# Performance work log

Hardware: AMD Instinct MI355X
Metric: run time of the kernel (lower is better)

Reference implementation:

```python
import jax, jax.numpy as jnp
import numpy as np

DIM = 256      # model dim E
H = 8          # num_heads
M = 32         # ball_size
TOPK = 2       # selected balls per query
N = 256        # number of balls
NM = N * M     # total points (8192)


def setup_inputs() -> dict:
    key = jax.random.key(0)
    k1, k2 = jax.random.split(key)
    x = jax.random.normal(k1, (NM, DIM), dtype=jnp.float32)
    pos = jax.random.normal(k2, (NM, 3), dtype=jnp.float32)
    return {"x": x, "pos": pos}


def reference(x, pos):
    e = DIM // H                      # per-head dim
    scale = DIM ** (-0.5)             # note: module scales by full dim, not head dim
    # pe_proj(compute_rel_pos(pos)) == 0 in the source (dead code), so x is unchanged.
    # qkv repeat + decompose '(H E K)' makes q == k == v == x reshaped per head.
    xh = x.reshape(N, M, H, e).transpose(0, 2, 1, 3)   # (n, H, m, e)
    q = xh
    k = xh
    v = xh

    # --- select_balls (runs under torch.no_grad) ---
    qf = jax.lax.stop_gradient(q).transpose(1, 0, 2, 3).reshape(H, NM, e)   # (H, nm, e)
    kmean = jax.lax.stop_gradient(k).mean(axis=2).transpose(1, 0, 2)        # (H, n, e)
    sim = jax.nn.softmax(jnp.einsum('hqe,hne->hqn', qf, kmean) * scale, axis=-1)
    topv, topi = jax.lax.top_k(sim, TOPK)               # (H, nm, topk)

    # straight-through gates (values were computed under no_grad -> constant 1.0)
    gates = topv + jax.lax.stop_gradient(1.0 - topv)
    # mask: each topk slot repeated over the m leaves of its ball
    fmask = jnp.repeat(topv > 1e-10, M, axis=-1)        # (H, nm, topk*m)

    # --- gather selected balls (avoid the torch repeat-then-gather blowup) ---
    kh = k.transpose(1, 0, 2, 3)                        # (H, n, m, e)
    vh = v.transpose(1, 0, 2, 3)
    gather = jax.vmap(lambda t, i: t[i])                # per-head fancy gather
    ksel = gather(kh, topi)                             # (H, nm, topk, m, e)
    vsel = gather(vh, topi)
    ksel = gates[..., None, None] * ksel                # use_diff_topk=True
    ksel = ksel.reshape(H, NM, TOPK * M, e)
    vsel = vsel.reshape(H, NM, TOPK * M, e)

    # --- masked attention over gathered keys ---
    qq = q.transpose(1, 0, 2, 3).reshape(H, NM, e)      # (H, nm, e)
    fsim = jnp.einsum('hqe,hqse->hqs', qq, ksel) * scale
    fsim = jnp.where(fmask, fsim, -jnp.finfo(fsim.dtype).max)
    attn = jax.nn.softmax(fsim, axis=-1)
    out = jnp.einsum('hqs,hqse->hqe', attn, vsel)       # (H, nm, e)
    return out.transpose(1, 0, 2).reshape(NM, DIM)      # (nm, H*e)
```

## Files before the change

kernel.cpp:

```cpp
#include <hip/hip_runtime.h>

#define FLT_BIG 3.402823466e38f

static __device__ __forceinline__ bool better(float v1, int i1, float v2, int i2) {
  return (v1 > v2) || ((v1 == v2) && (i1 < i2));
}

static __device__ __forceinline__ int xcd_swizzle(int nblocks) {
  const int bid = blockIdx.x;
  const int chunk = nblocks >> 3;
  return (bid & 7) * chunk + (bid >> 3);
}

__global__ void kmeanT_kernel(const float* __restrict__ x, float* __restrict__ kmT) {
  const int n = blockIdx.x;
  const int t = threadIdx.x;
  const float* base = x + n * 32 * 256 + t;
  float acc = 0.f;
  #pragma unroll
  for (int j = 0; j < 32; ++j) acc += base[j * 256];
  const int h = t >> 5, e = t & 31;
  kmT[h * 8192 + e * 256 + n] = acc * (1.0f / 32.0f);
}

__global__ __launch_bounds__(256) void select_kernel(const float* __restrict__ x,
                                                     const float* __restrict__ kmT,
                                                     int2* __restrict__ sel) {
  __shared__ float smem[32 * 260];
  const int vb = xcd_swizzle(2048);
  const int h = vb >> 8;
  const int qg = vb & 255;
  const int t = threadIdx.x;
  const int w = t >> 6, lane = t & 63;

  {
    const int r = t >> 3, c = t & 7;
    *(float4*)&smem[r * 32 + c * 4] =
        *(const float4*)(x + (qg * 32 + r) * 256 + h * 32 + c * 4);
  }
  __syncthreads();

  const float4* kmp = (const float4*)(kmT + h * 8192);
  float acc[8][4];
  #pragma unroll
  for (int qq = 0; qq < 8; ++qq)
    #pragma unroll
    for (int j = 0; j < 4; ++j) acc[qq][j] = 0.f;

  {
    float4 ka[4], kb[4];
    #pragma unroll
    for (int d = 0; d < 4; ++d) ka[d] = kmp[d * 64 + lane];

    #pragma unroll
    for (int e0 = 0; e0 < 8; ++e0) {
      float4* cur = (e0 & 1) ? kb : ka;
      float4* nxt = (e0 & 1) ? ka : kb;
      if (e0 < 7) {
        #pragma unroll
        for (int d = 0; d < 4; ++d) nxt[d] = kmp[((e0 + 1) * 4 + d) * 64 + lane];
      }
      #pragma unroll
      for (int qq = 0; qq < 8; ++qq) {
        const float4 qf = *(const float4*)&smem[(w * 8 + qq) * 32 + e0 * 4];
        acc[qq][0] = fmaf(qf.w, cur[3].x, fmaf(qf.z, cur[2].x, fmaf(qf.y, cur[1].x, fmaf(qf.x, cur[0].x, acc[qq][0]))));
        acc[qq][1] = fmaf(qf.w, cur[3].y, fmaf(qf.z, cur[2].y, fmaf(qf.y, cur[1].y, fmaf(qf.x, cur[0].y, acc[qq][1]))));
        acc[qq][2] = fmaf(qf.w, cur[3].z, fmaf(qf.z, cur[2].z, fmaf(qf.y, cur[1].z, fmaf(qf.x, cur[0].z, acc[qq][2]))));
        acc[qq][3] = fmaf(qf.w, cur[3].w, fmaf(qf.z, cur[2].w, fmaf(qf.y, cur[1].w, fmaf(qf.x, cur[0].w, acc[qq][3]))));
      }
    }
  }
  __syncthreads();

  #pragma unroll
  for (int qq = 0; qq < 8; ++qq) {
    *(float4*)&smem[(w * 8 + qq) * 260 + lane * 4] =
        make_float4(acc[qq][0], acc[qq][1], acc[qq][2], acc[qq][3]);
  }
  __syncthreads();

  const int qloc = t >> 3, ch = t & 7;
  const float* rowp = &smem[qloc * 260 + ch * 32];
  float a1 = -FLT_BIG, a2 = -FLT_BIG;
  int j1 = 0, j2 = 0;
  #pragma unroll
  for (int i = 0; i < 8; ++i) {
    const float4 v4 = *(const float4*)(rowp + i * 4);
    const int b0 = ch * 32 + i * 4;
    if (v4.x > a1) { a2 = a1; j2 = j1; a1 = v4.x; j1 = b0; }
    else if (v4.x > a2) { a2 = v4.x; j2 = b0; }
    if (v4.y > a1) { a2 = a1; j2 = j1; a1 = v4.y; j1 = b0 + 1; }
    else if (v4.y > a2) { a2 = v4.y; j2 = b0 + 1; }
    if (v4.z > a1) { a2 = a1; j2 = j1; a1 = v4.z; j1 = b0 + 2; }
    else if (v4.z > a2) { a2 = v4.z; j2 = b0 + 2; }
    if (v4.w > a1) { a2 = a1; j2 = j1; a1 = v4.w; j1 = b0 + 3; }
    else if (v4.w > a2) { a2 = v4.w; j2 = b0 + 3; }
  }

  int pk = j1 | (j2 << 16);
  #pragma unroll
  for (int m = 1; m <= 4; m <<= 1) {
    const float b1 = __shfl_xor(a1, m);
    const float b2 = __shfl_xor(a2, m);
    const int bpk = __shfl_xor(pk, m);
    const int bj1 = bpk & 65535, bj2 = bpk >> 16;
    int c1 = pk & 65535, c2 = pk >> 16;
    if (better(b1, bj1, a1, c1)) {
      if (better(a1, c1, b2, bj2)) { a2 = a1; c2 = c1; } else { a2 = b2; c2 = bj2; }
      a1 = b1; c1 = bj1;
    } else if (better(b1, bj1, a2, c2)) { a2 = b1; c2 = bj1; }
    pk = c1 | (c2 << 16);
  }

  if (ch == 0) {
    sel[h * 8192 + qg * 32 + qloc] = make_int2(pk & 65535, pk >> 16);
  }
}

__global__ __launch_bounds__(256) void attn_kernel(const float* __restrict__ x,
                                                   const int2* __restrict__ sel,
                                                   float* __restrict__ out) {
  const int lane = threadIdx.x & 63;
  const int widx = threadIdx.x >> 6;
  const int task = xcd_swizzle(16384) * 4 + widx;
  const int h = task >> 13;
  const int q = task & 8191;
  const int o = lane & 7;
  const int ro = lane >> 3;

  const int2 sv = sel[task];
  const int bA = sv.x, bB = sv.y;

  const float4 qf = *(const float4*)(x + q * 256 + h * 32 + o * 4);

  float4 kA[4], kB[4];
  const float* xa = x + bA * 8192 + ro * 256 + h * 32 + o * 4;
  const float* xb = x + bB * 8192 + ro * 256 + h * 32 + o * 4;
  #pragma unroll
  for (int i = 0; i < 4; ++i) {
    kA[i] = *(const float4*)(xa + i * 2048);
    kB[i] = *(const float4*)(xb + i * 2048);
  }

  float dA[4], dB[4];
  #pragma unroll
  for (int i = 0; i < 4; ++i) {
    float a = qf.x * kA[i].x; a = fmaf(qf.y, kA[i].y, a);
    a = fmaf(qf.z, kA[i].z, a); a = fmaf(qf.w, kA[i].w, a);
    dA[i] = a;
    float b = qf.x * kB[i].x; b = fmaf(qf.y, kB[i].y, b);
    b = fmaf(qf.z, kB[i].z, b); b = fmaf(qf.w, kB[i].w, b);
    dB[i] = b;
  }
  #pragma unroll
  for (int m = 1; m <= 4; m <<= 1) {
    #pragma unroll
    for (int i = 0; i < 4; ++i) {
      dA[i] += __shfl_xor(dA[i], m);
      dB[i] += __shfl_xor(dB[i], m);
    }
  }

  float pA[4], pB[4], psum = 0.f;
  #pragma unroll
  for (int i = 0; i < 4; ++i) {
    pA[i] = __expf(dA[i] * 0.0625f);
    pB[i] = __expf(dB[i] * 0.0625f);
    psum += pA[i] + pB[i];
  }
  #pragma unroll
  for (int m = 8; m <= 32; m <<= 1) psum += __shfl_xor(psum, m);

  float ox = 0.f, oy = 0.f, oz = 0.f, ow = 0.f;
  #pragma unroll
  for (int i = 0; i < 4; ++i) {
    ox = fmaf(pA[i], kA[i].x, ox); oy = fmaf(pA[i], kA[i].y, oy);
    oz = fmaf(pA[i], kA[i].z, oz); ow = fmaf(pA[i], kA[i].w, ow);
    ox = fmaf(pB[i], kB[i].x, ox); oy = fmaf(pB[i], kB[i].y, oy);
    oz = fmaf(pB[i], kB[i].z, oz); ow = fmaf(pB[i], kB[i].w, ow);
  }
  #pragma unroll
  for (int m = 8; m <= 32; m <<= 1) {
    ox += __shfl_xor(ox, m);
    oy += __shfl_xor(oy, m);
    oz += __shfl_xor(oz, m);
    ow += __shfl_xor(ow, m);
  }

  const float inv = 1.0f / psum;
  if (ro == 0) {
    *(float4*)(out + q * 256 + h * 32 + o * 4) =
        make_float4(ox * inv, oy * inv, oz * inv, ow * inv);
  }
}

extern "C" void kernel_launch(void* const* d_in, const int* in_sizes, int n_in,
                              void* d_out, int out_size, void* d_ws, size_t ws_size,
                              hipStream_t stream) {
  const float* x = (const float*)d_in[0];
  float* kmT = (float*)d_ws;
  int2* sel = (int2*)((char*)d_ws + 262144);
  float* out = (float*)d_out;

  kmeanT_kernel<<<256, 256, 0, stream>>>(x, kmT);
  select_kernel<<<2048, 256, 0, stream>>>(x, kmT, sel);
  attn_kernel<<<16384, 256, 0, stream>>>(x, sel, out);
}
```

Baseline: 58.63 us.

## Fuse ball selection and gathered attention into one kernel

Merges the select and attention kernels so each block computes top-2 ball indices for its 32 queries and then, one query at a time per wave, runs the gathered attention using the query tile already in shared memory. This removes one kernel launch, the sel round-trip through global memory, and the reload of query vectors. In exchange, the attention work per block becomes a serial loop of 8 queries per wave, with far fewer blocks (2048 instead of 16384), which may reduce latency hiding for the scattered key gathers. The shared buffer is also split into separate qtile and simbuf arrays, which drops one barrier.

```diff
diff --git a/kernel.cpp b/kernel.cpp
--- a/kernel.cpp
+++ b/kernel.cpp
@@ -23,10 +23,11 @@
   kmT[h * 8192 + e * 256 + n] = acc * (1.0f / 32.0f);
 }
 
-__global__ __launch_bounds__(256) void select_kernel(const float* __restrict__ x,
-                                                     const float* __restrict__ kmT,
-                                                     int2* __restrict__ sel) {
-  __shared__ float smem[32 * 260];
+__global__ __launch_bounds__(256) void fused_kernel(const float* __restrict__ x,
+                                                    const float* __restrict__ kmT,
+                                                    float* __restrict__ out) {
+  __shared__ float qtile[32 * 32];
+  __shared__ float simbuf[32 * 260];
   const int vb = xcd_swizzle(2048);
   const int h = vb >> 8;
   const int qg = vb & 255;
@@ -35,7 +36,7 @@
 
   {
     const int r = t >> 3, c = t & 7;
-    *(float4*)&smem[r * 32 + c * 4] =
+    *(float4*)&qtile[r * 32 + c * 4] =
         *(const float4*)(x + (qg * 32 + r) * 256 + h * 32 + c * 4);
   }
   __syncthreads();
@@ -62,7 +63,7 @@
       }
       #pragma unroll
       for (int qq = 0; qq < 8; ++qq) {
-        const float4 qf = *(const float4*)&smem[(w * 8 + qq) * 32 + e0 * 4];
+        const float4 qf = *(const float4*)&qtile[(w * 8 + qq) * 32 + e0 * 4];
         acc[qq][0] = fmaf(qf.w, cur[3].x, fmaf(qf.z, cur[2].x, fmaf(qf.y, cur[1].x, fmaf(qf.x, cur[0].x, acc[qq][0]))));
         acc[qq][1] = fmaf(qf.w, cur[3].y, fmaf(qf.z, cur[2].y, fmaf(qf.y, cur[1].y, fmaf(qf.x, cur[0].y, acc[qq][1]))));
         acc[qq][2] = fmaf(qf.w, cur[3].z, fmaf(qf.z, cur[2].z, fmaf(qf.y, cur[1].z, fmaf(qf.x, cur[0].z, acc[qq][2]))));
@@ -70,127 +71,118 @@
       }
     }
   }
-  __syncthreads();
 
   #pragma unroll
   for (int qq = 0; qq < 8; ++qq) {
-    *(float4*)&smem[(w * 8 + qq) * 260 + lane * 4] =
+    *(float4*)&simbuf[(w * 8 + qq) * 260 + lane * 4] =
         make_float4(acc[qq][0], acc[qq][1], acc[qq][2], acc[qq][3]);
   }
   __syncthreads();
 
-  const int qloc = t >> 3, ch = t & 7;
-  const float* rowp = &smem[qloc * 260 + ch * 32];
-  float a1 = -FLT_BIG, a2 = -FLT_BIG;
-  int j1 = 0, j2 = 0;
-  #pragma unroll
-  for (int i = 0; i < 8; ++i) {
-    const float4 v4 = *(const float4*)(rowp + i * 4);
-    const int b0 = ch * 32 + i * 4;
-    if (v4.x > a1) { a2 = a1; j2 = j1; a1 = v4.x; j1 = b0; }
-    else if (v4.x > a2) { a2 = v4.x; j2 = b0; }
-    if (v4.y > a1) { a2 = a1; j2 = j1; a1 = v4.y; j1 = b0 + 1; }
-    else if (v4.y > a2) { a2 = v4.y; j2 = b0 + 1; }
-    if (v4.z > a1) { a2 = a1; j2 = j1; a1 = v4.z; j1 = b0 + 2; }
-    else if (v4.z > a2) { a2 = v4.z; j2 = b0 + 2; }
-    if (v4.w > a1) { a2 = a1; j2 = j1; a1 = v4.w; j1 = b0 + 3; }
-    else if (v4.w > a2) { a2 = v4.w; j2 = b0 + 3; }
-  }
+  int pk;
+  {
+    const int qloc = t >> 3, ch = t & 7;
+    const float* rowp = &simbuf[qloc * 260 + ch * 32];
+    float a1 = -FLT_BIG, a2 = -FLT_BIG;
+    int j1 = 0, j2 = 0;
+    #pragma unroll
+    for (int i = 0; i < 8; ++i) {
+      const float4 v4 = *(const float4*)(rowp + i * 4);
+      const int b0 = ch * 32 + i * 4;
+      if (v4.x > a1) { a2 = a1; j2 = j1; a1 = v4.x; j1 = b0; }
+      else if (v4.x > a2) { a2 = v4.x; j2 = b0; }
+      if (v4.y > a1) { a2 = a1; j2 = j1; a1 = v4.y; j1 = b0 + 1; }
+      else if (v4.y > a2) { a2 = v4.y; j2 = b0 + 1; }
+      if (v4.z > a1) { a2 = a1; j2 = j1; a1 = v4.z; j1 = b0 + 2; }
+      else if (v4.z > a2) { a2 = v4.z; j2 = b0 + 2; }
+      if (v4.w > a1) { a2 = a1; j2 = j1; a1 = v4.w; j1 = b0 + 3; }
+      else if (v4.w > a2) { a2 = v4.w; j2 = b0 + 3; }
+    }
 
-  int pk = j1 | (j2 << 16);
-  #pragma unroll
-  for (int m = 1; m <= 4; m <<= 1) {
-    const float b1 = __shfl_xor(a1, m);
-    const float b2 = __shfl_xor(a2, m);
-    const int bpk = __shfl_xor(pk, m);
-    const int bj1 = bpk & 65535, bj2 = bpk >> 16;
-    int c1 = pk & 65535, c2 = pk >> 16;
-    if (better(b1, bj1, a1, c1)) {
-      if (better(a1, c1, b2, bj2)) { a2 = a1; c2 = c1; } else { a2 = b2; c2 = bj2; }
-      a1 = b1; c1 = bj1;
-    } else if (better(b1, bj1, a2, c2)) { a2 = b1; c2 = bj1; }
-    pk = c1 | (c2 << 16);
-  }
-
-  if (ch == 0) {
-    sel[h * 8192 + qg * 32 + qloc] = make_int2(pk & 65535, pk >> 16);
-  }
-}
-
-__global__ __launch_bounds__(256) void attn_kernel(const float* __restrict__ x,
-                                                   const int2* __restrict__ sel,
-                                                   float* __restrict__ out) {
-  const int lane = threadIdx.x & 63;
-  const int widx = threadIdx.x >> 6;
-  const int task = xcd_swizzle(16384) * 4 + widx;
-  const int h = task >> 13;
-  const int q = task & 8191;
-  const int o = lane & 7;
-  const int ro = lane >> 3;
-
-  const int2 sv = sel[task];
-  const int bA = sv.x, bB = sv.y;
-
-  const float4 qf = *(const float4*)(x + q * 256 + h * 32 + o * 4);
-
-  float4 kA[4], kB[4];
-  const float* xa = x + bA * 8192 + ro * 256 + h * 32 + o * 4;
-  const float* xb = x + bB * 8192 + ro * 256 + h * 32 + o * 4;
-  #pragma unroll
-  for (int i = 0; i < 4; ++i) {
-    kA[i] = *(const float4*)(xa + i * 2048);
-    kB[i] = *(const float4*)(xb + i * 2048);
-  }
-
-  float dA[4], dB[4];
-  #pragma unroll
-  for (int i = 0; i < 4; ++i) {
-    float a = qf.x * kA[i].x; a = fmaf(qf.y, kA[i].y, a);
-    a = fmaf(qf.z, kA[i].z, a); a = fmaf(qf.w, kA[i].w, a);
-    dA[i] = a;
-    float b = qf.x * kB[i].x; b = fmaf(qf.y, kB[i].y, b);
-    b = fmaf(qf.z, kB[i].z, b); b = fmaf(qf.w, kB[i].w, b);
-    dB[i] = b;
-  }
-  #pragma unroll
-  for (int m = 1; m <= 4; m <<= 1) {
+    pk = j1 | (j2 << 16);
     #pragma unroll
-    for (int i = 0; i < 4; ++i) {
-      dA[i] += __shfl_xor(dA[i], m);
-      dB[i] += __shfl_xor(dB[i], m);
+    for (int m = 1; m <= 4; m <<= 1) {
+      const float b1 = __shfl_xor(a1, m);
+      const float b2 = __shfl_xor(a2, m);
+      const int bpk = __shfl_xor(pk, m);
+      const int bj1 = bpk & 65535, bj2 = bpk >> 16;
+      int c1 = pk & 65535, c2 = pk >> 16;
+      if (better(b1, bj1, a1, c1)) {
+        if (better(a1, c1, b2, bj2)) { a2 = a1; c2 = c1; } else { a2 = b2; c2 = bj2; }
+        a1 = b1; c1 = bj1;
+      } else if (better(b1, bj1, a2, c2)) { a2 = b1; c2 = bj1; }
+      pk = c1 | (c2 << 16);
     }
   }
 
-  float pA[4], pB[4], psum = 0.f;
-  #pragma unroll
-  for (int i = 0; i < 4; ++i) {
-    pA[i] = __expf(dA[i] * 0.0625f);
-    pB[i] = __expf(dB[i] * 0.0625f);
-    psum += pA[i] + pB[i];
-  }
-  #pragma unroll
-  for (int m = 8; m <= 32; m <<= 1) psum += __shfl_xor(psum, m);
+  const int o = lane & 7;
+  const int ro = lane >> 3;
+  #pragma unroll 1
+  for (int qq = 0; qq < 8; ++qq) {
+    const int qloc = w * 8 + qq;
+    const int pkq = __shfl(pk, qq * 8);
+    const int bA = pkq & 65535, bB = pkq >> 16;
+    const float4 qf = *(const float4*)&qtile[qloc * 32 + o * 4];
 
-  float ox = 0.f, oy = 0.f, oz = 0.f, ow = 0.f;
-  #pragma unroll
-  for (int i = 0; i < 4; ++i) {
-    ox = fmaf(pA[i], kA[i].x, ox); oy = fmaf(pA[i], kA[i].y, oy);
-    oz = fmaf(pA[i], kA[i].z, oz); ow = fmaf(pA[i], kA[i].w, ow);
-    ox = fmaf(pB[i], kB[i].x, ox); oy = fmaf(pB[i], kB[i].y, oy);
-    oz = fmaf(pB[i], kB[i].z, oz); ow = fmaf(pB[i], kB[i].w, ow);
-  }
-  #pragma unroll
-  for (int m = 8; m <= 32; m <<= 1) {
-    ox += __shfl_xor(ox, m);
-    oy += __shfl_xor(oy, m);
-    oz += __shfl_xor(oz, m);
-    ow += __shfl_xor(ow, m);
-  }
+    float4 kA[4], kB[4];
+    const float* xa = x + bA * 8192 + ro * 256 + h * 32 + o * 4;
+    const float* xb = x + bB * 8192 + ro * 256 + h * 32 + o * 4;
+    #pragma unroll
+    for (int i = 0; i < 4; ++i) {
+      kA[i] = *(const float4*)(xa + i * 2048);
+      kB[i] = *(const float4*)(xb + i * 2048);
+    }
 
-  const float inv = 1.0f / psum;
-  if (ro == 0) {
-    *(float4*)(out + q * 256 + h * 32 + o * 4) =
-        make_float4(ox * inv, oy * inv, oz * inv, ow * inv);
+    float dA[4], dB[4];
+    #pragma unroll
+    for (int i = 0; i < 4; ++i) {
+      float a = qf.x * kA[i].x; a = fmaf(qf.y, kA[i].y, a);
+      a = fmaf(qf.z, kA[i].z, a); a = fmaf(qf.w, kA[i].w, a);
+      dA[i] = a;
+      float b = qf.x * kB[i].x; b = fmaf(qf.y, kB[i].y, b);
+      b = fmaf(qf.z, kB[i].z, b); b = fmaf(qf.w, kB[i].w, b);
+      dB[i] = b;
+    }
+    #pragma unroll
+    for (int m = 1; m <= 4; m <<= 1) {
+      #pragma unroll
+      for (int i = 0; i < 4; ++i) {
+        dA[i] += __shfl_xor(dA[i], m);
+        dB[i] += __shfl_xor(dB[i], m);
+      }
+    }
+
+    float pA[4], pB[4], psum = 0.f;
+    #pragma unroll
+    for (int i = 0; i < 4; ++i) {
+      pA[i] = __expf(dA[i] * 0.0625f);
+      pB[i] = __expf(dB[i] * 0.0625f);
+      psum += pA[i] + pB[i];
+    }
+    #pragma unroll
+    for (int m = 8; m <= 32; m <<= 1) psum += __shfl_xor(psum, m);
+
+    float ox = 0.f, oy = 0.f, oz = 0.f, ow = 0.f;
+    #pragma unroll
+    for (int i = 0; i < 4; ++i) {
+      ox = fmaf(pA[i], kA[i].x, ox); oy = fmaf(pA[i], kA[i].y, oy);
+      oz = fmaf(pA[i], kA[i].z, oz); ow = fmaf(pA[i], kA[i].w, ow);
+      ox = fmaf(pB[i], kB[i].x, ox); oy = fmaf(pB[i], kB[i].y, oy);
+      oz = fmaf(pB[i], kB[i].z, oz); ow = fmaf(pB[i], kB[i].w, ow);
+    }
+    #pragma unroll
+    for (int m = 8; m <= 32; m <<= 1) {
+      ox += __shfl_xor(ox, m);
+      oy += __shfl_xor(oy, m);
+      oz += __shfl_xor(oz, m);
+      ow += __shfl_xor(ow, m);
+    }
+
+    const float inv = 1.0f / psum;
+    if (ro == 0) {
+      *(float4*)(out + (qg * 32 + qloc) * 256 + h * 32 + o * 4) =
+          make_float4(ox * inv, oy * inv, oz * inv, ow * inv);
+    }
   }
 }
 
@@ -199,10 +191,8 @@
                               hipStream_t stream) {
   const float* x = (const float*)d_in[0];
   float* kmT = (float*)d_ws;
-  int2* sel = (int2*)((char*)d_ws + 262144);
   float* out = (float*)d_out;
 
   kmeanT_kernel<<<256, 256, 0, stream>>>(x, kmT);
-  select_kernel<<<2048, 256, 0, stream>>>(x, kmT, sel);
-  attn_kernel<<<16384, 256, 0, stream>>>(x, sel, out);
+  fused_kernel<<<2048, 256, 0, stream>>>(x, kmT, out);
 }
```

Result: faster. 57.34 us (-2.2%).
